# Kernel tuning notes

Measured on AMD Instinct MI355X. Metric: run time of the kernel, lower is better.

The kernel has to match this reference:

```python
import jax, jax.numpy as jnp
import numpy as np

N_NODES = 100000
N_EDGES = 600000
N_GRAPHS = 512


def _glorot(key, shape):
    fan_in, fan_out = shape
    lim = np.sqrt(6.0 / (fan_in + fan_out)).astype(np.float32)
    return jax.random.uniform(key, shape, jnp.float32, -lim, lim)


def setup_inputs() -> dict:
    key = jax.random.key(0)
    ks = jax.random.split(key, 12)
    x = jax.random.normal(ks[0], (N_NODES, 3), jnp.float32)
    edge_index = jax.random.randint(ks[1], (2, N_EDGES), 0, N_NODES, jnp.int64)
    batch = jnp.sort(jax.random.randint(ks[2], (N_NODES,), 0, N_GRAPHS, jnp.int64))
    return {
        "x": x,
        "edge_index": edge_index,
        "batch": batch,
        "W1": _glorot(ks[3], (3, 128)),   "b1": jnp.zeros((128,), jnp.float32),
        "W2": _glorot(ks[4], (128, 128)), "b2": jnp.zeros((128,), jnp.float32),
        "W3": _glorot(ks[5], (128, 64)),  "b3": jnp.zeros((64,), jnp.float32),
        "Wl": _glorot(ks[6], (64, 1)),    "bl": jnp.zeros((1,), jnp.float32),
    }


def _gcn_conv(h, W, b, src, dst, deg_inv_sqrt):
    # linear transform, then normalized gather-scatter aggregation (self-loops
    # already included in src/dst and deg_inv_sqrt).
    h = h @ W                                            # [N, F_out]
    norm = deg_inv_sqrt[src] * deg_inv_sqrt[dst]         # [E+N]
    msg = h[src] * norm[:, None]                         # [E+N, F_out]
    out = jax.ops.segment_sum(msg, dst, num_segments=N_NODES)
    return out + b


def reference(x, edge_index, batch, W1, b1, W2, b2, W3, b3, Wl, bl):
    # add self-loops (GCNConv default add_self_loops=True)
    loop = jnp.arange(N_NODES, dtype=edge_index.dtype)
    src = jnp.concatenate([edge_index[0], loop])
    dst = jnp.concatenate([edge_index[1], loop])
    # symmetric normalization deg^{-1/2} (in-degree at target, edge weight 1)
    deg = jax.ops.segment_sum(jnp.ones_like(dst, jnp.float32), dst,
                              num_segments=N_NODES)
    deg_inv_sqrt = jnp.where(deg > 0, jax.lax.rsqrt(jnp.maximum(deg, 1.0)), 0.0)

    h = jax.nn.relu(_gcn_conv(x, W1, b1, src, dst, deg_inv_sqrt))
    h = jax.nn.relu(_gcn_conv(h, W2, b2, src, dst, deg_inv_sqrt))
    h = jax.nn.relu(_gcn_conv(h, W3, b3, src, dst, deg_inv_sqrt))

    # global mean pool over graphs
    sums = jax.ops.segment_sum(h, batch, num_segments=N_GRAPHS)    # [G, 64]
    counts = jax.ops.segment_sum(jnp.ones((N_NODES,), jnp.float32), batch,
                                 num_segments=N_GRAPHS)
    pooled = sums / jnp.maximum(counts, 1.0)[:, None]

    return pooled @ Wl + bl                                        # [G, 1]
```

## Files before the change

kernel.cpp:

```cpp
#include <hip/hip_runtime.h>

#define N_NODES 100000
#define N_EDGES 600000
#define N_GRAPHS 512

typedef __attribute__((ext_vector_type(8))) short short8;
typedef __attribute__((ext_vector_type(4))) float floatx4;

__device__ __forceinline__ unsigned short f2bf(float f) {
    unsigned int u = __float_as_uint(f);
    u += 0x7FFFu + ((u >> 16) & 1u);
    return (unsigned short)(u >> 16);
}
__device__ __forceinline__ float bf_lo(unsigned int u) { return __uint_as_float(u << 16); }
__device__ __forceinline__ float bf_hi(unsigned int u) { return __uint_as_float(u & 0xFFFF0000u); }

__device__ __forceinline__ void fma8(float* a, short8 v, float n) {
    union { short8 s; unsigned int u[4]; } c; c.s = v;
    #pragma unroll
    for (int j = 0; j < 4; ++j) {
        a[2 * j]     = fmaf(bf_lo(c.u[j]), n, a[2 * j]);
        a[2 * j + 1] = fmaf(bf_hi(c.u[j]), n, a[2 * j + 1]);
    }
}
__device__ __forceinline__ void init8(float* a, short8 v, float s) {
    union { short8 s; unsigned int u[4]; } c; c.s = v;
    #pragma unroll
    for (int j = 0; j < 4; ++j) {
        a[2 * j]     = bf_lo(c.u[j]) * s;
        a[2 * j + 1] = bf_hi(c.u[j]) * s;
    }
}
__device__ __forceinline__ short8 pack8(const float* a) {
    short8 r;
    #pragma unroll
    for (int j = 0; j < 8; ++j) r[j] = (short)f2bf(a[j]);
    return r;
}

__global__ void k_hist(const int* __restrict__ dst, int* cnt) {
    int e = blockIdx.x * 256 + threadIdx.x;
    if (e < N_EDGES) atomicAdd(&cnt[dst[e]], 1);
}

__global__ void k_scan1(const int* __restrict__ cnt, int* __restrict__ part) {
    __shared__ int s[256];
    int t = threadIdx.x;
    int i = blockIdx.x * 256 + t;
    int v = (i < N_NODES) ? cnt[i] : 0;
    s[t] = v; __syncthreads();
    for (int off = 128; off > 0; off >>= 1) {
        if (t < off) s[t] += s[t + off];
        __syncthreads();
    }
    if (t == 0) part[blockIdx.x] = s[0];
}

__global__ void k_scan3(const int* __restrict__ cnt, const int* __restrict__ part,
                        int* __restrict__ row_ptr, int* __restrict__ cursor,
                        float* __restrict__ dis) {
    __shared__ int s[256];
    __shared__ int pbaseS;
    int t = threadIdx.x;
    int psum = 0;
    for (int k = t; k < blockIdx.x; k += 256) psum += part[k];
    s[t] = psum; __syncthreads();
    for (int off = 128; off > 0; off >>= 1) {
        if (t < off) s[t] += s[t + off];
        __syncthreads();
    }
    if (t == 0) pbaseS = s[0];
    __syncthreads();
    int pbase = pbaseS;
    __syncthreads();
    int i = blockIdx.x * 256 + t;
    int v = (i < N_NODES) ? cnt[i] : 0;
    s[t] = v; __syncthreads();
    for (int off = 1; off < 256; off <<= 1) {
        int u = (t >= off) ? s[t - off] : 0;
        __syncthreads();
        s[t] += u;
        __syncthreads();
    }
    int ex = s[t] - v + pbase;
    if (i < N_NODES) {
        row_ptr[i] = ex; cursor[i] = ex;
        dis[i] = 1.0f / sqrtf((float)(v + 1));
    }
    if (blockIdx.x == 0 && t == 0) row_ptr[N_NODES] = N_EDGES;
}

__global__ void k_scatter(const int* __restrict__ src, const int* __restrict__ dst,
                          const float* __restrict__ dis, int* __restrict__ cursor,
                          int* __restrict__ csr_src, float* __restrict__ csr_norm) {
    int e = blockIdx.x * 256 + threadIdx.x;
    if (e >= N_EDGES) return;
    int s = src[e], d = dst[e];
    int pos = atomicAdd(&cursor[d], 1);
    csr_src[pos] = s;
    csr_norm[pos] = dis[s] * dis[d];
}

__device__ __forceinline__ void pack_one(const float* __restrict__ W, unsigned short* __restrict__ out,
                                         int idx, int N) {
    int lane = idx & 63;
    int ks = (idx >> 6) & 3;
    int ct = idx >> 8;
    int n = ct * 16 + (lane & 15);
    int kbase = ks * 32 + (lane >> 4) * 8;
    #pragma unroll
    for (int j = 0; j < 8; ++j)
        out[(size_t)idx * 8 + j] = f2bf(W[(size_t)(kbase + j) * N + n]);
}

#define NB1 6250
__global__ __launch_bounds__(256) void k_node1(const float* __restrict__ x,
                                               const float* __restrict__ dis,
                                               const int* __restrict__ row_ptr,
                                               const int* __restrict__ csr_src,
                                               const float* __restrict__ csr_norm,
                                               const float* __restrict__ W1,
                                               const float* __restrict__ b1,
                                               unsigned short* __restrict__ out,
                                               const float* __restrict__ W2,
                                               const float* __restrict__ W3,
                                               unsigned short* __restrict__ Wp2,
                                               unsigned short* __restrict__ Wp3) {
    int tid = threadIdx.x;
    if (blockIdx.x >= NB1) {
        int idx = (blockIdx.x - NB1) * 256 + tid;
        if (idx < 2048) pack_one(W2, Wp2, idx, 128);
        else if (idx < 3072) pack_one(W3, Wp3, idx - 2048, 64);
        return;
    }
    __shared__ float Ws[384];
    __shared__ float bs[128];
    for (int i = tid; i < 384; i += 256) Ws[i] = W1[i];
    if (tid < 128) bs[tid] = b1[tid];
    __syncthreads();
    int gw = (blockIdx.x * 256 + tid) >> 6;
    int lane = tid & 63;
    int sub = lane >> 4, l16 = lane & 15;
    int node = gw * 4 + sub;
    int beg = row_ptr[node], end = row_ptr[node + 1];
    float p0 = 0.f, p1 = 0.f, p2 = 0.f;
    for (int e = beg + l16; e < end; e += 16) {
        int s = csr_src[e];
        float n = csr_norm[e];
        p0 = fmaf(x[s * 3 + 0], n, p0);
        p1 = fmaf(x[s * 3 + 1], n, p1);
        p2 = fmaf(x[s * 3 + 2], n, p2);
    }
    #pragma unroll
    for (int m = 8; m > 0; m >>= 1) {
        p0 += __shfl_xor(p0, m, 64);
        p1 += __shfl_xor(p1, m, 64);
        p2 += __shfl_xor(p2, m, 64);
    }
    float d = dis[node], s2 = d * d;
    float a0 = fmaf(x[node * 3 + 0], s2, p0);
    float a1 = fmaf(x[node * 3 + 1], s2, p1);
    float a2 = fmaf(x[node * 3 + 2], s2, p2);
    int f = l16 * 8;
    float v[8];
    #pragma unroll
    for (int j = 0; j < 8; ++j)
        v[j] = fmaxf(bs[f + j] + a0 * Ws[f + j] + a1 * Ws[128 + f + j] + a2 * Ws[256 + f + j], 0.f);
    *(short8*)(out + (size_t)node * 128 + f) = pack8(v);
}

__global__ __launch_bounds__(256) void k_layer23(const unsigned short* __restrict__ h1,
                                                 const float* __restrict__ dis,
                                                 const int* __restrict__ row_ptr,
                                                 const int* __restrict__ csr_src,
                                                 const float* __restrict__ csr_norm,
                                                 const unsigned short* __restrict__ Wp2,
                                                 const float* __restrict__ b2,
                                                 const unsigned short* __restrict__ Wp3,
                                                 unsigned short* __restrict__ Q2b) {
    __shared__ unsigned short Asb[32][136];
    __shared__ unsigned short Hsb[32][136];
    int tid = threadIdx.x;
    int wave = tid >> 6, lane = tid & 63;
    int quad = lane >> 4, m16 = lane & 15;
    int base = blockIdx.x * 32;

    {
        int sub = lane >> 4, l16 = lane & 15;
        int rA = wave * 8 + sub, rB = rA + 4;
        int nodeA = base + rA, nodeB = base + rB;
        int begA = row_ptr[nodeA], endA = row_ptr[nodeA + 1];
        int begB = row_ptr[nodeB], endB = row_ptr[nodeB + 1];
        int idxA[8], idxB[8]; float nnA[8], nnB[8];
        #pragma unroll
        for (int u = 0; u < 8; ++u) {
            int ee = begA + u; int cl = ee < endA ? ee : endA - 1;
            idxA[u] = csr_src[cl]; nnA[u] = ee < endA ? csr_norm[cl] : 0.0f;
        }
        #pragma unroll
        for (int u = 0; u < 8; ++u) {
            int ee = begB + u; int cl = ee < endB ? ee : endB - 1;
            idxB[u] = csr_src[cl]; nnB[u] = ee < endB ? csr_norm[cl] : 0.0f;
        }
        float dA = dis[nodeA], dB = dis[nodeB];
        short8 selfA = *(const short8*)(h1 + (size_t)nodeA * 128 + l16 * 8);
        short8 selfB = *(const short8*)(h1 + (size_t)nodeB * 128 + l16 * 8);

        short8 gA[8], gB[8];
        #pragma unroll
        for (int u = 0; u < 8; ++u)
            gA[u] = *(const short8*)(h1 + (size_t)idxA[u] * 128 + l16 * 8);
        #pragma unroll
        for (int u = 0; u < 8; ++u)
            gB[u] = *(const short8*)(h1 + (size_t)idxB[u] * 128 + l16 * 8);

        float aA[8], aB[8];
        init8(aA, selfA, dA * dA);
        #pragma unroll
        for (int u = 0; u < 8; ++u) fma8(aA, gA[u], nnA[u]);
        init8(aB, selfB, dB * dB);
        #pragma unroll
        for (int u = 0; u < 8; ++u) fma8(aB, gB[u], nnB[u]);

        for (int e = begA + 8; e < endA; e += 8) {
            int idx[8]; float nn[8];
            #pragma unroll
            for (int u = 0; u < 8; ++u) {
                int ee = e + u; int cl = ee < endA ? ee : endA - 1;
                idx[u] = csr_src[cl]; nn[u] = ee < endA ? csr_norm[cl] : 0.0f;
            }
            short8 g[8];
            #pragma unroll
            for (int u = 0; u < 8; ++u)
                g[u] = *(const short8*)(h1 + (size_t)idx[u] * 128 + l16 * 8);
            #pragma unroll
            for (int u = 0; u < 8; ++u) fma8(aA, g[u], nn[u]);
        }
        *(short8*)(&Asb[rA][l16 * 8]) = pack8(aA);

        for (int e = begB + 8; e < endB; e += 8) {
            int idx[8]; float nn[8];
            #pragma unroll
            for (int u = 0; u < 8; ++u) {
                int ee = e + u; int cl = ee < endB ? ee : endB - 1;
                idx[u] = csr_src[cl]; nn[u] = ee < endB ? csr_norm[cl] : 0.0f;
            }
            short8 g[8];
            #pragma unroll
            for (int u = 0; u < 8; ++u)
                g[u] = *(const short8*)(h1 + (size_t)idx[u] * 128 + l16 * 8);
            #pragma unroll
            for (int u = 0; u < 8; ++u) fma8(aB, g[u], nn[u]);
        }
        *(short8*)(&Asb[rB][l16 * 8]) = pack8(aB);
    }
    __syncthreads();

    int mt = wave & 1;
    int ch = wave >> 1;
    {
        short8 af[4];
        #pragma unroll
        for (int ks = 0; ks < 4; ++ks)
            af[ks] = *(const short8*)(&Asb[mt * 16 + m16][ks * 32 + quad * 8]);
        floatx4 acc[4];
        #pragma unroll
        for (int ct = 0; ct < 4; ++ct) acc[ct] = (floatx4){0.f, 0.f, 0.f, 0.f};
        #pragma unroll
        for (int ct = 0; ct < 4; ++ct) {
            int gct = ch * 4 + ct;
            #pragma unroll
            for (int ks = 0; ks < 4; ++ks) {
                short8 bf = *(const short8*)(Wp2 + ((size_t)(gct * 4 + ks) * 64 + lane) * 8);
                acc[ct] = __builtin_amdgcn_mfma_f32_16x16x32_bf16(af[ks], bf, acc[ct], 0, 0, 0);
            }
        }
        #pragma unroll
        for (int ct = 0; ct < 4; ++ct) {
            int col = (ch * 4 + ct) * 16 + m16;
            float bv = b2[col];
            #pragma unroll
            for (int r = 0; r < 4; ++r) {
                int row = mt * 16 + quad * 4 + r;
                Hsb[row][col] = f2bf(fmaxf(acc[ct][r] + bv, 0.0f));
            }
        }
    }
    __syncthreads();

    {
        int cp = wave >> 1;
        short8 hf[4];
        #pragma unroll
        for (int ks = 0; ks < 4; ++ks)
            hf[ks] = *(const short8*)(&Hsb[mt * 16 + m16][ks * 32 + quad * 8]);
        floatx4 acc3[2];
        acc3[0] = (floatx4){0.f, 0.f, 0.f, 0.f};
        acc3[1] = (floatx4){0.f, 0.f, 0.f, 0.f};
        #pragma unroll
        for (int ct = 0; ct < 2; ++ct) {
            int gct = cp * 2 + ct;
            #pragma unroll
            for (int ks = 0; ks < 4; ++ks) {
                short8 bf = *(const short8*)(Wp3 + ((size_t)(gct * 4 + ks) * 64 + lane) * 8);
                acc3[ct] = __builtin_amdgcn_mfma_f32_16x16x32_bf16(hf[ks], bf, acc3[ct], 0, 0, 0);
            }
        }
        #pragma unroll
        for (int ct = 0; ct < 2; ++ct) {
            int col = (cp * 2 + ct) * 16 + m16;
            #pragma unroll
            for (int r = 0; r < 4; ++r) {
                long row = base + mt * 16 + quad * 4 + r;
                Q2b[row * 64 + col] = f2bf(acc3[ct][r]);
            }
        }
    }
}

__global__ __launch_bounds__(256) void k_agg64_dot(const unsigned short* __restrict__ h,
                                                   const float* __restrict__ dis,
                                                   const int* __restrict__ row_ptr,
                                                   const int* __restrict__ csr_src,
                                                   const float* __restrict__ csr_norm,
                                                   const float* __restrict__ bias,
                                                   const float* __restrict__ Wl,
                                                   float* __restrict__ s_out) {
    int gw = (blockIdx.x * 256 + threadIdx.x) >> 6;
    int lane = threadIdx.x & 63;
    int sub = lane >> 3, l8 = lane & 7;
    int node = gw * 8 + sub;
    int beg = row_ptr[node], end = row_ptr[node + 1];
    int idx[8]; float nn[8];
    #pragma unroll
    for (int u = 0; u < 8; ++u) {
        int ee = beg + u; int cl = ee < end ? ee : end - 1;
        idx[u] = csr_src[cl]; nn[u] = ee < end ? csr_norm[cl] : 0.0f;
    }
    float d = dis[node];
    short8 self = *(const short8*)(h + (size_t)node * 64 + l8 * 8);
    short8 g[8];
    #pragma unroll
    for (int u = 0; u < 8; ++u)
        g[u] = *(const short8*)(h + (size_t)idx[u] * 64 + l8 * 8);
    float a[8];
    init8(a, self, d * d);
    #pragma unroll
    for (int u = 0; u < 8; ++u) fma8(a, g[u], nn[u]);
    for (int e = beg + 8; e < end; e += 8) {
        int idx2[8]; float nn2[8];
        #pragma unroll
        for (int u = 0; u < 8; ++u) {
            int ee = e + u; int cl = ee < end ? ee : end - 1;
            idx2[u] = csr_src[cl]; nn2[u] = ee < end ? csr_norm[cl] : 0.0f;
        }
        short8 g2[8];
        #pragma unroll
        for (int u = 0; u < 8; ++u)
            g2[u] = *(const short8*)(h + (size_t)idx2[u] * 64 + l8 * 8);
        #pragma unroll
        for (int u = 0; u < 8; ++u) fma8(a, g2[u], nn2[u]);
    }
    int f = l8 * 8;
    float v = 0.f;
    #pragma unroll
    for (int j = 0; j < 8; ++j)
        v = fmaf(fmaxf(a[j] + bias[f + j], 0.f), Wl[f + j], v);
    #pragma unroll
    for (int m = 4; m > 0; m >>= 1) v += __shfl_xor(v, m, 64);
    if (l8 == 0) s_out[node] = v;
}

__global__ __launch_bounds__(256) void k_pool2(const float* __restrict__ s,
                                               const int* __restrict__ batch,
                                               const float* __restrict__ bl,
                                               float* __restrict__ out) {
    int g = blockIdx.x;
    int tid = threadIdx.x;
    int lo = 0, hi = N_NODES;
    while (lo < hi) { int m = (lo + hi) >> 1; if (batch[m] < g) lo = m + 1; else hi = m; }
    int lo2 = lo, hi2 = N_NODES;
    while (lo2 < hi2) { int m = (lo2 + hi2) >> 1; if (batch[m] < g + 1) lo2 = m + 1; else hi2 = m; }
    float acc = 0.0f;
    for (int n = lo + tid; n < lo2; n += 256) acc += s[n];
    __shared__ float sm[256];
    sm[tid] = acc; __syncthreads();
    for (int off = 128; off > 0; off >>= 1) {
        if (tid < off) sm[tid] += sm[tid + off];
        __syncthreads();
    }
    if (tid == 0) out[g] = sm[0] / fmaxf((float)(lo2 - lo), 1.0f) + bl[0];
}

extern "C" void kernel_launch(void* const* d_in, const int* in_sizes, int n_in,
                              void* d_out, int out_size, void* d_ws, size_t ws_size,
                              hipStream_t stream) {
    const float* x     = (const float*)d_in[0];
    const int*   ei    = (const int*)d_in[1];
    const int*   batch = (const int*)d_in[2];
    const float* W1 = (const float*)d_in[3];
    const float* b1 = (const float*)d_in[4];
    const float* W2 = (const float*)d_in[5];
    const float* b2 = (const float*)d_in[6];
    const float* W3 = (const float*)d_in[7];
    const float* b3 = (const float*)d_in[8];
    const float* Wl = (const float*)d_in[9];
    const float* bl = (const float*)d_in[10];
    float* out = (float*)d_out;

    const int* e_src = ei;
    const int* e_dst = ei + N_EDGES;

    char* ws = (char*)d_ws;
    size_t off = 0;
    auto alloc = [&](size_t bytes) -> char* {
        char* p = ws + off;
        off = (off + bytes + 255) & ~(size_t)255;
        return p;
    };
    int*   cnt      = (int*)  alloc((size_t)N_NODES * 4);
    float* dis      = (float*)alloc((size_t)N_NODES * 4);
    int*   row_ptr  = (int*)  alloc((size_t)(N_NODES + 1) * 4);
    int*   cursor   = (int*)  alloc((size_t)N_NODES * 4);
    int*   part     = (int*)  alloc(1024 * 4);
    int*   csr_src  = (int*)  alloc((size_t)N_EDGES * 4);
    float* csr_norm = (float*)alloc((size_t)N_EDGES * 4);
    float* nscal    = (float*)alloc((size_t)N_NODES * 4);
    unsigned short* P1b = (unsigned short*)alloc((size_t)N_NODES * 128 * 2);
    unsigned short* Q2b = (unsigned short*)alloc((size_t)N_NODES * 64 * 2);
    unsigned short* Wp2 = (unsigned short*)alloc((size_t)128 * 128 * 2);
    unsigned short* Wp3 = (unsigned short*)alloc((size_t)128 * 64 * 2);

    const int NB_N = (N_NODES + 255) / 256;
    const int NB_E = (N_EDGES + 255) / 256;

    hipMemsetAsync(cnt, 0, (size_t)N_NODES * 4, stream);
    k_hist<<<NB_E, 256, 0, stream>>>(e_dst, cnt);
    k_scan1<<<NB_N, 256, 0, stream>>>(cnt, part);
    k_scan3<<<NB_N, 256, 0, stream>>>(cnt, part, row_ptr, cursor, dis);
    k_scatter<<<NB_E, 256, 0, stream>>>(e_src, e_dst, dis, cursor, csr_src, csr_norm);

    k_node1<<<NB1 + 12, 256, 0, stream>>>(x, dis, row_ptr, csr_src, csr_norm,
                                          W1, b1, P1b, W2, W3, Wp2, Wp3);

    k_layer23<<<N_NODES / 32, 256, 0, stream>>>(P1b, dis, row_ptr, csr_src, csr_norm,
                                                Wp2, b2, Wp3, Q2b);

    k_agg64_dot<<<N_NODES / 8 / 4, 256, 0, stream>>>(Q2b, dis, row_ptr, csr_src, csr_norm,
                                                     b3, Wl, nscal);

    k_pool2<<<N_GRAPHS, 256, 0, stream>>>(nscal, batch, bl, out);
}
```

Baseline: 217.9 us.

## Halve layer23 block tile and fuse pooling into aggregation via atomics

k_layer23 now handles 16 nodes per block instead of 32, with one node per 16-lane group. This doubles the grid and cuts per-thread register and LDS use, trading more weight reloads per block for occupancy. Per-node scalars are no longer written out and re-read by a pool kernel. They are atomically added into per-graph sums, and a tiny final kernel divides by the counts. The atomics may contend, since the batch indices are sorted, and the float summation order becomes nondeterministic.

```diff
diff --git a/kernel.cpp b/kernel.cpp
--- a/kernel.cpp
+++ b/kernel.cpp
@@ -178,142 +178,98 @@
                                                  const float* __restrict__ b2,
                                                  const unsigned short* __restrict__ Wp3,
                                                  unsigned short* __restrict__ Q2b) {
-    __shared__ unsigned short Asb[32][136];
-    __shared__ unsigned short Hsb[32][136];
+    __shared__ unsigned short Asb[16][136];
+    __shared__ unsigned short Hsb[16][136];
     int tid = threadIdx.x;
     int wave = tid >> 6, lane = tid & 63;
     int quad = lane >> 4, m16 = lane & 15;
-    int base = blockIdx.x * 32;
+    int base = blockIdx.x * 16;
 
     {
         int sub = lane >> 4, l16 = lane & 15;
-        int rA = wave * 8 + sub, rB = rA + 4;
-        int nodeA = base + rA, nodeB = base + rB;
-        int begA = row_ptr[nodeA], endA = row_ptr[nodeA + 1];
-        int begB = row_ptr[nodeB], endB = row_ptr[nodeB + 1];
-        int idxA[8], idxB[8]; float nnA[8], nnB[8];
+        int r = wave * 4 + sub;
+        int node = base + r;
+        int beg = row_ptr[node], end = row_ptr[node + 1];
+        int idx[8]; float nn[8];
         #pragma unroll
         for (int u = 0; u < 8; ++u) {
-            int ee = begA + u; int cl = ee < endA ? ee : endA - 1;
-            idxA[u] = csr_src[cl]; nnA[u] = ee < endA ? csr_norm[cl] : 0.0f;
-        }
-        #pragma unroll
-        for (int u = 0; u < 8; ++u) {
-            int ee = begB + u; int cl = ee < endB ? ee : endB - 1;
-            idxB[u] = csr_src[cl]; nnB[u] = ee < endB ? csr_norm[cl] : 0.0f;
-        }
-        float dA = dis[nodeA], dB = dis[nodeB];
-        short8 selfA = *(const short8*)(h1 + (size_t)nodeA * 128 + l16 * 8);
-        short8 selfB = *(const short8*)(h1 + (size_t)nodeB * 128 + l16 * 8);
-
-        short8 gA[8], gB[8];
+            int ee = beg + u; int cl = ee < end ? ee : end - 1;
+            idx[u] = csr_src[cl]; nn[u] = ee < end ? csr_norm[cl] : 0.0f;
+        }
+        float d = dis[node];
+        short8 self = *(const short8*)(h1 + (size_t)node * 128 + l16 * 8);
+        short8 g[8];
         #pragma unroll
         for (int u = 0; u < 8; ++u)
-            gA[u] = *(const short8*)(h1 + (size_t)idxA[u] * 128 + l16 * 8);
-        #pragma unroll
-        for (int u = 0; u < 8; ++u)
-            gB[u] = *(const short8*)(h1 + (size_t)idxB[u] * 128 + l16 * 8);
-
-        float aA[8], aB[8];
-        init8(aA, selfA, dA * dA);
-        #pragma unroll
-        for (int u = 0; u < 8; ++u) fma8(aA, gA[u], nnA[u]);
-        init8(aB, selfB, dB * dB);
-        #pragma unroll
-        for (int u = 0; u < 8; ++u) fma8(aB, gB[u], nnB[u]);
-
-        for (int e = begA + 8; e < endA; e += 8) {
-            int idx[8]; float nn[8];
+            g[u] = *(const short8*)(h1 + (size_t)idx[u] * 128 + l16 * 8);
+        float a[8];
+        init8(a, self, d * d);
+        #pragma unroll
+        for (int u = 0; u < 8; ++u) fma8(a, g[u], nn[u]);
+        for (int e = beg + 8; e < end; e += 8) {
+            int idx2[8]; float nn2[8];
             #pragma unroll
             for (int u = 0; u < 8; ++u) {
-                int ee = e + u; int cl = ee < endA ? ee : endA - 1;
-                idx[u] = csr_src[cl]; nn[u] = ee < endA ? csr_norm[cl] : 0.0f;
+                int ee = e + u; int cl = ee < end ? ee : end - 1;
+                idx2[u] = csr_src[cl]; nn2[u] = ee < end ? csr_norm[cl] : 0.0f;
             }
-            short8 g[8];
+            short8 g2[8];
             #pragma unroll
             for (int u = 0; u < 8; ++u)
-                g[u] = *(const short8*)(h1 + (size_t)idx[u] * 128 + l16 * 8);
+                g2[u] = *(const short8*)(h1 + (size_t)idx2[u] * 128 + l16 * 8);
             #pragma unroll
-            for (int u = 0; u < 8; ++u) fma8(aA, g[u], nn[u]);
-        }
-        *(short8*)(&Asb[rA][l16 * 8]) = pack8(aA);
-
-        for (int e = begB + 8; e < endB; e += 8) {
-            int idx[8]; float nn[8];
-            #pragma unroll
-            for (int u = 0; u < 8; ++u) {
-                int ee = e + u; int cl = ee < endB ? ee : endB - 1;
-                idx[u] = csr_src[cl]; nn[u] = ee < endB ? csr_norm[cl] : 0.0f;
-            }
-            short8 g[8];
-            #pragma unroll
-            for (int u = 0; u < 8; ++u)
-                g[u] = *(const short8*)(h1 + (size_t)idx[u] * 128 + l16 * 8);
-            #pragma unroll
-            for (int u = 0; u < 8; ++u) fma8(aB, g[u], nn[u]);
-        }
-        *(short8*)(&Asb[rB][l16 * 8]) = pack8(aB);
+            for (int u = 0; u < 8; ++u) fma8(a, g2[u], nn2[u]);
+        }
+        *(short8*)(&Asb[r][l16 * 8]) = pack8(a);
     }
     __syncthreads();
 
-    int mt = wave & 1;
-    int ch = wave >> 1;
     {
         short8 af[4];
         #pragma unroll
         for (int ks = 0; ks < 4; ++ks)
-            af[ks] = *(const short8*)(&Asb[mt * 16 + m16][ks * 32 + quad * 8]);
-        floatx4 acc[4];
-        #pragma unroll
-        for (int ct = 0; ct < 4; ++ct) acc[ct] = (floatx4){0.f, 0.f, 0.f, 0.f};
-        #pragma unroll
-        for (int ct = 0; ct < 4; ++ct) {
-            int gct = ch * 4 + ct;
+            af[ks] = *(const short8*)(&Asb[m16][ks * 32 + quad * 8]);
+        floatx4 acc[2];
+        acc[0] = (floatx4){0.f, 0.f, 0.f, 0.f};
+        acc[1] = (floatx4){0.f, 0.f, 0.f, 0.f};
+        #pragma unroll
+        for (int c = 0; c < 2; ++c) {
+            int gct = wave * 2 + c;
             #pragma unroll
             for (int ks = 0; ks < 4; ++ks) {
                 short8 bf = *(const short8*)(Wp2 + ((size_t)(gct * 4 + ks) * 64 + lane) * 8);
-                acc[ct] = __builtin_amdgcn_mfma_f32_16x16x32_bf16(af[ks], bf, acc[ct], 0, 0, 0);
+                acc[c] = __builtin_amdgcn_mfma_f32_16x16x32_bf16(af[ks], bf, acc[c], 0, 0, 0);
             }
         }
         #pragma unroll
-        for (int ct = 0; ct < 4; ++ct) {
-            int col = (ch * 4 + ct) * 16 + m16;
+        for (int c = 0; c < 2; ++c) {
+            int col = (wave * 2 + c) * 16 + m16;
             float bv = b2[col];
             #pragma unroll
             for (int r = 0; r < 4; ++r) {
-                int row = mt * 16 + quad * 4 + r;
-                Hsb[row][col] = f2bf(fmaxf(acc[ct][r] + bv, 0.0f));
+                int row = quad * 4 + r;
+                Hsb[row][col] = f2bf(fmaxf(acc[c][r] + bv, 0.0f));
             }
         }
     }
     __syncthreads();
 
     {
-        int cp = wave >> 1;
         short8 hf[4];
         #pragma unroll
         for (int ks = 0; ks < 4; ++ks)
-            hf[ks] = *(const short8*)(&Hsb[mt * 16 + m16][ks * 32 + quad * 8]);
-        floatx4 acc3[2];
-        acc3[0] = (floatx4){0.f, 0.f, 0.f, 0.f};
-        acc3[1] = (floatx4){0.f, 0.f, 0.f, 0.f};
-        #pragma unroll
-        for (int ct = 0; ct < 2; ++ct) {
-            int gct = cp * 2 + ct;
-            #pragma unroll
-            for (int ks = 0; ks < 4; ++ks) {
-                short8 bf = *(const short8*)(Wp3 + ((size_t)(gct * 4 + ks) * 64 + lane) * 8);
-                acc3[ct] = __builtin_amdgcn_mfma_f32_16x16x32_bf16(hf[ks], bf, acc3[ct], 0, 0, 0);
-            }
-        }
-        #pragma unroll
-        for (int ct = 0; ct < 2; ++ct) {
-            int col = (cp * 2 + ct) * 16 + m16;
-            #pragma unroll
-            for (int r = 0; r < 4; ++r) {
-                long row = base + mt * 16 + quad * 4 + r;
-                Q2b[row * 64 + col] = f2bf(acc3[ct][r]);
-            }
+            hf[ks] = *(const short8*)(&Hsb[m16][ks * 32 + quad * 8]);
+        floatx4 acc3 = (floatx4){0.f, 0.f, 0.f, 0.f};
+        #pragma unroll
+        for (int ks = 0; ks < 4; ++ks) {
+            short8 bf = *(const short8*)(Wp3 + ((size_t)(wave * 4 + ks) * 64 + lane) * 8);
+            acc3 = __builtin_amdgcn_mfma_f32_16x16x32_bf16(hf[ks], bf, acc3, 0, 0, 0);
+        }
+        int col = wave * 16 + m16;
+        #pragma unroll
+        for (int r = 0; r < 4; ++r) {
+            long row = base + quad * 4 + r;
+            Q2b[row * 64 + col] = f2bf(acc3[r]);
         }
     }
 }
@@ -325,7 +281,8 @@
                                                    const float* __restrict__ csr_norm,
                                                    const float* __restrict__ bias,
                                                    const float* __restrict__ Wl,
-                                                   float* __restrict__ s_out) {
+                                                   const int* __restrict__ batch,
+                                                   float* __restrict__ gsum) {
     int gw = (blockIdx.x * 256 + threadIdx.x) >> 6;
     int lane = threadIdx.x & 63;
     int sub = lane >> 3, l8 = lane & 7;
@@ -368,28 +325,20 @@
         v = fmaf(fmaxf(a[j] + bias[f + j], 0.f), Wl[f + j], v);
     #pragma unroll
     for (int m = 4; m > 0; m >>= 1) v += __shfl_xor(v, m, 64);
-    if (l8 == 0) s_out[node] = v;
-}
-
-__global__ __launch_bounds__(256) void k_pool2(const float* __restrict__ s,
+    if (l8 == 0) atomicAdd(&gsum[batch[node]], v);
+}
+
+__global__ __launch_bounds__(256) void k_final(const float* __restrict__ gsum,
                                                const int* __restrict__ batch,
                                                const float* __restrict__ bl,
                                                float* __restrict__ out) {
-    int g = blockIdx.x;
-    int tid = threadIdx.x;
+    int g = blockIdx.x * 256 + threadIdx.x;
+    if (g >= N_GRAPHS) return;
     int lo = 0, hi = N_NODES;
     while (lo < hi) { int m = (lo + hi) >> 1; if (batch[m] < g) lo = m + 1; else hi = m; }
     int lo2 = lo, hi2 = N_NODES;
     while (lo2 < hi2) { int m = (lo2 + hi2) >> 1; if (batch[m] < g + 1) lo2 = m + 1; else hi2 = m; }
-    float acc = 0.0f;
-    for (int n = lo + tid; n < lo2; n += 256) acc += s[n];
-    __shared__ float sm[256];
-    sm[tid] = acc; __syncthreads();
-    for (int off = 128; off > 0; off >>= 1) {
-        if (tid < off) sm[tid] += sm[tid + off];
-        __syncthreads();
-    }
-    if (tid == 0) out[g] = sm[0] / fmaxf((float)(lo2 - lo), 1.0f) + bl[0];
+    out[g] = gsum[g] / fmaxf((float)(lo2 - lo), 1.0f) + bl[0];
 }
 
 extern "C" void kernel_launch(void* const* d_in, const int* in_sizes, int n_in,
@@ -419,13 +368,13 @@
         return p;
     };
     int*   cnt      = (int*)  alloc((size_t)N_NODES * 4);
+    float* gsum     = (float*)alloc((size_t)N_GRAPHS * 4);
     float* dis      = (float*)alloc((size_t)N_NODES * 4);
     int*   row_ptr  = (int*)  alloc((size_t)(N_NODES + 1) * 4);
     int*   cursor   = (int*)  alloc((size_t)N_NODES * 4);
     int*   part     = (int*)  alloc(1024 * 4);
     int*   csr_src  = (int*)  alloc((size_t)N_EDGES * 4);
     float* csr_norm = (float*)alloc((size_t)N_EDGES * 4);
-    float* nscal    = (float*)alloc((size_t)N_NODES * 4);
     unsigned short* P1b = (unsigned short*)alloc((size_t)N_NODES * 128 * 2);
     unsigned short* Q2b = (unsigned short*)alloc((size_t)N_NODES * 64 * 2);
     unsigned short* Wp2 = (unsigned short*)alloc((size_t)128 * 128 * 2);
@@ -434,7 +383,7 @@
     const int NB_N = (N_NODES + 255) / 256;
     const int NB_E = (N_EDGES + 255) / 256;
 
-    hipMemsetAsync(cnt, 0, (size_t)N_NODES * 4, stream);
+    hipMemsetAsync(cnt, 0, (size_t)((char*)gsum - (char*)cnt) + (size_t)N_GRAPHS * 4, stream);
     k_hist<<<NB_E, 256, 0, stream>>>(e_dst, cnt);
     k_scan1<<<NB_N, 256, 0, stream>>>(cnt, part);
     k_scan3<<<NB_N, 256, 0, stream>>>(cnt, part, row_ptr, cursor, dis);
@@ -443,11 +392,11 @@
     k_node1<<<NB1 + 12, 256, 0, stream>>>(x, dis, row_ptr, csr_src, csr_norm,
                                           W1, b1, P1b, W2, W3, Wp2, Wp3);
 
-    k_layer23<<<N_NODES / 32, 256, 0, stream>>>(P1b, dis, row_ptr, csr_src, csr_norm,
+    k_layer23<<<N_NODES / 16, 256, 0, stream>>>(P1b, dis, row_ptr, csr_src, csr_norm,
                                                 Wp2, b2, Wp3, Q2b);
 
     k_agg64_dot<<<N_NODES / 8 / 4, 256, 0, stream>>>(Q2b, dis, row_ptr, csr_src, csr_norm,
-                                                     b3, Wl, nscal);
-
-    k_pool2<<<N_GRAPHS, 256, 0, stream>>>(nscal, batch, bl, out);
-}
+                                                     b3, Wl, batch, gsum);
+
+    k_final<<<(N_GRAPHS + 255) / 256, 256, 0, stream>>>(gsum, batch, bl, out);
+}
```

After: 358.8 us. 1.65x slower.
